# Kernel optimization log

Hardware: AMD Instinct MI355X
Metric: run time of the kernel (lower is better)

Reference implementation:

```python
import jax, jax.numpy as jnp
import numpy as np
from jax import lax

NUM_LAYERS = 3
NUM_QUBITS = 8
BATCH = 131072
DIM = 2 ** NUM_QUBITS  # 256


def _rot_mats(params):
    # params: (L, Q, 3) angles for RX, RY, RZ. Returns combined U = RZ @ RY @ RX, (L, Q, 2, 2) complex64.
    half = params * 0.5
    cx = jnp.cos(half[..., 0]).astype(jnp.complex64)
    sx = jnp.sin(half[..., 0]).astype(jnp.complex64)
    cy = jnp.cos(half[..., 1]).astype(jnp.complex64)
    sy = jnp.sin(half[..., 1]).astype(jnp.complex64)
    ezm = jnp.exp(-1j * half[..., 2]).astype(jnp.complex64)
    ezp = jnp.exp(1j * half[..., 2]).astype(jnp.complex64)
    zero = jnp.zeros_like(cx)
    RX = jnp.stack([jnp.stack([cx, -1j * sx], -1), jnp.stack([-1j * sx, cx], -1)], -2)
    RY = jnp.stack([jnp.stack([cy, -sy], -1), jnp.stack([sy, cy], -1)], -2)
    RZ = jnp.stack([jnp.stack([ezm, zero], -1), jnp.stack([zero, ezp], -1)], -2)
    return jnp.einsum('lqij,lqjk,lqkm->lqim', RZ, RY, RX)


def _apply_1q(state, U, wire):
    # state: (B, 2,2,...,2); wire w lives on axis w+1 (PennyLane wire 0 = most significant bit)
    ax = wire + 1
    return jnp.moveaxis(jnp.tensordot(U, state, axes=((1,), (ax,))), 0, ax)


def _apply_cnot(state, ctrl, tgt):
    c_ax, t_ax = ctrl + 1, tgt + 1
    s0 = lax.index_in_dim(state, 0, axis=c_ax, keepdims=True)
    s1 = lax.index_in_dim(state, 1, axis=c_ax, keepdims=True)
    s1 = jnp.flip(s1, axis=t_ax)
    return jnp.concatenate([s0, s1], axis=c_ax)


def _circuit(params, state_re, state_im):
    U = _rot_mats(params)  # (L, Q, 2, 2)
    state = (state_re + 1j * state_im).astype(jnp.complex64)
    state = state.reshape((state.shape[0],) + (2,) * NUM_QUBITS)
    for l in range(NUM_LAYERS):
        for q in range(NUM_QUBITS):
            state = _apply_1q(state, U[l, q], q)
        for q in range(NUM_QUBITS):
            state = _apply_cnot(state, q, (q + 1) % NUM_QUBITS)
    state = state.reshape(state.shape[0], DIM)
    # probability that wire 0 measures |0>: sum |amp|^2 over first half of amplitudes
    half = state[:, : DIM // 2]
    return jnp.sum(half.real ** 2 + half.imag ** 2, axis=1).astype(jnp.float32)


def setup_inputs() -> dict:
    key = jax.random.key(0)
    k1, k2, k3 = jax.random.split(key, 3)
    params = jax.random.uniform(k1, (NUM_LAYERS, NUM_QUBITS, 3), dtype=jnp.float32)
    sr = jax.random.normal(k2, (BATCH, DIM), dtype=jnp.float32)
    si = jax.random.normal(k3, (BATCH, DIM), dtype=jnp.float32)
    norm = jnp.sqrt(jnp.sum(sr ** 2 + si ** 2, axis=1, keepdims=True))
    return {"params": params, "state_re": sr / norm, "state_im": si / norm}


def reference(params, state_re, state_im):
    return _circuit(params, state_re, state_im)
```

## Files before the change

kernel.cpp:

```cpp
#include <hip/hip_runtime.h>
#include <stdint.h>

#define NLAYERS 3
#define NQ 8
#define DIM 256
#define BATCH 131072

typedef float  f32x4  __attribute__((ext_vector_type(4)));
typedef __bf16 bf16x8 __attribute__((ext_vector_type(8)));

__device__ __forceinline__ unsigned short f2bf(float f){
    union { float f; uint32_t u; } v; v.f = f;
    uint32_t u = v.u;
    u += 0x7fffu + ((u >> 16) & 1u);
    return (unsigned short)(u >> 16);
}

__device__ __forceinline__ float2 cmul(float2 a, float2 b){
    return make_float2(a.x*b.x - a.y*b.y, a.x*b.y + a.y*b.x);
}

__device__ __forceinline__ void gload_lds16(void* lds, const void* g){
    __builtin_amdgcn_global_load_lds(
        (const __attribute__((address_space(1))) unsigned int*)g,
        (__attribute__((address_space(3))) unsigned int*)lds,
        16, 0, 0);
}

__global__ __launch_bounds__(256) void build_w_kernel(const float* __restrict__ params,
                                                      unsigned short* __restrict__ W){
    __shared__ float2 st[2][DIM];
    __shared__ float2 gm[NLAYERS*NQ][4];
    const int j = blockIdx.x;
    const int i = threadIdx.x;

    if (i < NLAYERS*NQ){
        const float* pp = params + i*3;
        float hx = 0.5f*pp[0], hy = 0.5f*pp[1], hz = 0.5f*pp[2];
        float cx = cosf(hx), sx = sinf(hx);
        float cy = cosf(hy), sy = sinf(hy);
        float cz = cosf(hz), sz = sinf(hz);
        float2 ezm = make_float2(cz, -sz), ezp = make_float2(cz, sz);
        float2 m00 = make_float2( cy*cx,  sy*sx);
        float2 m01 = make_float2(-sy*cx, -cy*sx);
        float2 m10 = make_float2( sy*cx, -cy*sx);
        float2 m11 = make_float2( cy*cx, -sy*sx);
        gm[i][0] = cmul(ezm, m00);
        gm[i][1] = cmul(ezm, m01);
        gm[i][2] = cmul(ezp, m10);
        gm[i][3] = cmul(ezp, m11);
    }

    int psrc = i;
    #pragma unroll
    for (int q = NQ-1; q >= 0; --q){
        int c  = 7 - q;
        int tb = 7 - ((q + 1) & 7);
        psrc = ((psrc >> c) & 1) ? (psrc ^ (1 << tb)) : psrc;
    }

    int cur = 0;
    st[0][i] = make_float2(i == j ? 1.0f : 0.0f, 0.0f);
    __syncthreads();

    for (int l = 0; l < NLAYERS; ++l){
        for (int q = 0; q < NQ; ++q){
            float2 U0a = gm[l*NQ+q][0], U0b = gm[l*NQ+q][1];
            float2 U1a = gm[l*NQ+q][2], U1b = gm[l*NQ+q][3];
            int p  = 7 - q;
            int bs = (i >> p) & 1;
            int i0 = i & ~(1 << p), i1 = i | (1 << p);
            float2 a0 = st[cur][i0], a1 = st[cur][i1];
            float2 ua = bs ? U1a : U0a;
            float2 ub = bs ? U1b : U0b;
            float2 r;
            r.x = ua.x*a0.x - ua.y*a0.y + ub.x*a1.x - ub.y*a1.y;
            r.y = ua.x*a0.y + ua.y*a0.x + ub.x*a1.y + ub.y*a1.x;
            st[cur ^ 1][i] = r;
            cur ^= 1;
            __syncthreads();
        }
        float2 r = st[cur][psrc];
        st[cur ^ 1][i] = r;
        cur ^= 1;
        __syncthreads();
    }

    const int m = i & 127;
    float2 a = st[cur][m];
    if (i < 128) W[(uint32_t)m*256u + (uint32_t)j]          = f2bf(a.x);
    else         W[32768u + (uint32_t)m*256u + (uint32_t)j] = f2bf(a.y);
}


#define STAGE(B) { \
    gload_lds16(&Abuf[B][(c0+0)*DIM], srcp0); srcp0 += 16*DIM; \
    gload_lds16(&Abuf[B][(c0+1)*DIM], srcp1); srcp1 += 16*DIM; \
    gload_lds16(&Abuf[B][(c0+2)*DIM], srcp2); srcp2 += 16*DIM; \
    gload_lds16(&Abuf[B][(c0+3)*DIM], srcp3); srcp3 += 16*DIM; \
    gload_lds16(&Abuf[B][(c0+4)*DIM], srcp4); srcp4 += 16*DIM; \
    gload_lds16(&Abuf[B][(c0+5)*DIM], srcp5); srcp5 += 16*DIM; \
    gload_lds16(&Abuf[B][(c0+6)*DIM], srcp6); srcp6 += 16*DIM; \
    gload_lds16(&Abuf[B][(c0+7)*DIM], srcp7); srcp7 += 16*DIM; }

#define LOADB(F, S) \
    const bf16x8 bre_##F##_##S = *(const bf16x8*)(wrp##F + S*32); \
    const bf16x8 bim_##F##_##S = *(const bf16x8*)(wrp##F + 32768 + S*32);

#define BSTEP(S) { \
    f32x4 ra0 = *(const f32x4*)(arow + S*32 + o0); \
    f32x4 ra1 = *(const f32x4*)(arow + S*32 + o1); \
    f32x4 qa0 = *(const f32x4*)(irow + S*32 + o0); \
    f32x4 qa1 = *(const f32x4*)(irow + S*32 + o1); \
    union { f32x4 v; uint32_t u[4]; } ha_, hb_; \
    union { uint32_t u[4]; bf16x8 f; } pr_, pi_, pn_; \
    ha_.v = ra0; hb_.v = ra1; \
    pr_.u[0] = __builtin_amdgcn_perm(ha_.u[1], ha_.u[0], 0x07060302); \
    pr_.u[1] = __builtin_amdgcn_perm(ha_.u[3], ha_.u[2], 0x07060302); \
    pr_.u[2] = __builtin_amdgcn_perm(hb_.u[1], hb_.u[0], 0x07060302); \
    pr_.u[3] = __builtin_amdgcn_perm(hb_.u[3], hb_.u[2], 0x07060302); \
    ha_.v = qa0; hb_.v = qa1; \
    pi_.u[0] = __builtin_amdgcn_perm(ha_.u[1], ha_.u[0], 0x07060302); \
    pi_.u[1] = __builtin_amdgcn_perm(ha_.u[3], ha_.u[2], 0x07060302); \
    pi_.u[2] = __builtin_amdgcn_perm(hb_.u[1], hb_.u[0], 0x07060302); \
    pi_.u[3] = __builtin_amdgcn_perm(hb_.u[3], hb_.u[2], 0x07060302); \
    pn_.u[0] = pi_.u[0] ^ 0x80008000u; \
    pn_.u[1] = pi_.u[1] ^ 0x80008000u; \
    pn_.u[2] = pi_.u[2] ^ 0x80008000u; \
    pn_.u[3] = pi_.u[3] ^ 0x80008000u; \
    const bf16x8 fr_ = pr_.f, fi_ = pi_.f, fn_ = pn_.f; \
    accR0 = __builtin_amdgcn_mfma_f32_16x16x32_bf16(fr_, bre_0_##S, accR0, 0, 0, 0); \
    accR0 = __builtin_amdgcn_mfma_f32_16x16x32_bf16(fn_, bim_0_##S, accR0, 0, 0, 0); \
    accI0 = __builtin_amdgcn_mfma_f32_16x16x32_bf16(fr_, bim_0_##S, accI0, 0, 0, 0); \
    accI0 = __builtin_amdgcn_mfma_f32_16x16x32_bf16(fi_, bre_0_##S, accI0, 0, 0, 0); \
    accR1 = __builtin_amdgcn_mfma_f32_16x16x32_bf16(fr_, bre_1_##S, accR1, 0, 0, 0); \
    accR1 = __builtin_amdgcn_mfma_f32_16x16x32_bf16(fn_, bim_1_##S, accR1, 0, 0, 0); \
    accI1 = __builtin_amdgcn_mfma_f32_16x16x32_bf16(fr_, bim_1_##S, accI1, 0, 0, 0); \
    accI1 = __builtin_amdgcn_mfma_f32_16x16x32_bf16(fi_, bre_1_##S, accI1, 0, 0, 0); \
}

__global__ __launch_bounds__(256, 2) void qform4_kernel(const float* __restrict__ sr,
                                                        const float* __restrict__ si,
                                                        const unsigned short* __restrict__ W,
                                                        float* __restrict__ out){
    __shared__ float Abuf[2][32*DIM];
    __shared__ float red[64];

    const int tid  = threadIdx.x;
    const int lane = tid & 63;
    const int w    = tid >> 6;
    const int l15  = lane & 15;
    const int quad = lane >> 4;
    const int x7   = l15 & 7;
    const size_t m0 = (size_t)blockIdx.x * 128;

    const int c0 = w * 8;
    #define SRCP(I) ((((c0+I) < 16) ? sr : si) + (m0 + ((c0+I)&15))*DIM + ((lane ^ ((c0+I)&7)) << 2))
    const float* srcp0 = SRCP(0);
    const float* srcp1 = SRCP(1);
    const float* srcp2 = SRCP(2);
    const float* srcp3 = SRCP(3);
    const float* srcp4 = SRCP(4);
    const float* srcp5 = SRCP(5);
    const float* srcp6 = SRCP(6);
    const float* srcp7 = SRCP(7);
    #undef SRCP

    STAGE(0)

    const unsigned short* wrp0 = W + ((uint32_t)(w*32 +  0 + l15))*256u + (uint32_t)(quad*8);
    const unsigned short* wrp1 = W + ((uint32_t)(w*32 + 16 + l15))*256u + (uint32_t)(quad*8);
    LOADB(0,0) LOADB(0,1) LOADB(0,2) LOADB(0,3)
    LOADB(0,4) LOADB(0,5) LOADB(0,6) LOADB(0,7)
    LOADB(1,0) LOADB(1,1) LOADB(1,2) LOADB(1,3)
    LOADB(1,4) LOADB(1,5) LOADB(1,6) LOADB(1,7)

    const int o0 = (((quad << 1)    ) ^ x7) << 2;
    const int o1 = (((quad << 1) | 1) ^ x7) << 2;

    int buf = 0;
    #pragma unroll 1
    for (int t = 0; t < 8; ++t){
        if (t < 7){
            STAGE(buf ^ 1)
            asm volatile("s_waitcnt vmcnt(8)" ::: "memory");
        } else {
            asm volatile("s_waitcnt vmcnt(0)" ::: "memory");
        }
        __builtin_amdgcn_s_barrier();
        __builtin_amdgcn_sched_barrier(0);

        const float* arow = &Abuf[buf][l15 * DIM];
        const float* irow = &Abuf[buf][(16 + l15) * DIM];

        f32x4 accR0 = {0.f,0.f,0.f,0.f}, accI0 = {0.f,0.f,0.f,0.f};
        f32x4 accR1 = {0.f,0.f,0.f,0.f}, accI1 = {0.f,0.f,0.f,0.f};
        BSTEP(0) BSTEP(1) BSTEP(2) BSTEP(3)
        BSTEP(4) BSTEP(5) BSTEP(6) BSTEP(7)

        #pragma unroll
        for (int r = 0; r < 4; ++r){
            const float v0 = accR0[r], u0 = accI0[r];
            const float v1 = accR1[r], u1 = accI1[r];
            float tt = v0*v0 + u0*u0 + v1*v1 + u1*u1;
            tt += __shfl_xor(tt, 1);
            tt += __shfl_xor(tt, 2);
            tt += __shfl_xor(tt, 4);
            tt += __shfl_xor(tt, 8);
            if (l15 == 0) red[w*16 + quad*4 + r] = tt;
        }
        asm volatile("s_waitcnt lgkmcnt(0)" ::: "memory");
        __builtin_amdgcn_s_barrier();
        __builtin_amdgcn_sched_barrier(0);

        if (tid < 16){
            out[m0 + t*16 + tid] = red[tid] + red[16 + tid] + red[32 + tid] + red[48 + tid];
        }
        buf ^= 1;
    }
}

extern "C" void kernel_launch(void* const* d_in, const int* in_sizes, int n_in,
                              void* d_out, int out_size, void* d_ws, size_t ws_size,
                              hipStream_t stream){
    const float* params = (const float*)d_in[0];
    const float* sr     = (const float*)d_in[1];
    const float* si     = (const float*)d_in[2];
    unsigned short* Wimg = (unsigned short*)d_ws;
    float* out          = (float*)d_out;

    build_w_kernel<<<dim3(DIM), dim3(256), 0, stream>>>(params, Wimg);
    qform4_kernel<<<dim3(1024), dim3(256), 0, stream>>>(sr, si, Wimg, out);
}
```

Before: 301.8 us.

## Stage input tiles through registers and merge per-iteration barriers

Swaps the direct global-to-LDS async loads for ordinary vector loads into registers, which are then written to LDS after each compute step. The next tile's loads are issued one iteration ahead and land in the other LDS buffer. The reduction scratch array is double-buffered so each loop iteration needs only one workgroup barrier instead of two. The trade-off is extra VGPR pressure from holding eight float4 values per thread, plus explicit ds_write instructions in place of the hardware LDS-direct path.

```diff
diff --git a/kernel.cpp b/kernel.cpp
--- a/kernel.cpp
+++ b/kernel.cpp
@@ -18,13 +18,6 @@
 
 __device__ __forceinline__ float2 cmul(float2 a, float2 b){
     return make_float2(a.x*b.x - a.y*b.y, a.x*b.y + a.y*b.x);
-}
-
-__device__ __forceinline__ void gload_lds16(void* lds, const void* g){
-    __builtin_amdgcn_global_load_lds(
-        (const __attribute__((address_space(1))) unsigned int*)g,
-        (__attribute__((address_space(3))) unsigned int*)lds,
-        16, 0, 0);
 }
 
 __global__ __launch_bounds__(256) void build_w_kernel(const float* __restrict__ params,
@@ -93,15 +86,25 @@
 }
 
 
-#define STAGE(B) { \
-    gload_lds16(&Abuf[B][(c0+0)*DIM], srcp0); srcp0 += 16*DIM; \
-    gload_lds16(&Abuf[B][(c0+1)*DIM], srcp1); srcp1 += 16*DIM; \
-    gload_lds16(&Abuf[B][(c0+2)*DIM], srcp2); srcp2 += 16*DIM; \
-    gload_lds16(&Abuf[B][(c0+3)*DIM], srcp3); srcp3 += 16*DIM; \
-    gload_lds16(&Abuf[B][(c0+4)*DIM], srcp4); srcp4 += 16*DIM; \
-    gload_lds16(&Abuf[B][(c0+5)*DIM], srcp5); srcp5 += 16*DIM; \
-    gload_lds16(&Abuf[B][(c0+6)*DIM], srcp6); srcp6 += 16*DIM; \
-    gload_lds16(&Abuf[B][(c0+7)*DIM], srcp7); srcp7 += 16*DIM; }
+#define STAGE_ISSUE() { \
+    g0 = *(const f32x4*)srcp0; srcp0 += 16*DIM; \
+    g1 = *(const f32x4*)srcp1; srcp1 += 16*DIM; \
+    g2 = *(const f32x4*)srcp2; srcp2 += 16*DIM; \
+    g3 = *(const f32x4*)srcp3; srcp3 += 16*DIM; \
+    g4 = *(const f32x4*)srcp4; srcp4 += 16*DIM; \
+    g5 = *(const f32x4*)srcp5; srcp5 += 16*DIM; \
+    g6 = *(const f32x4*)srcp6; srcp6 += 16*DIM; \
+    g7 = *(const f32x4*)srcp7; srcp7 += 16*DIM; }
+
+#define DSWRITE(B) { \
+    *(f32x4*)(&Abuf[B][(c0+0)*DIM + (lane<<2)]) = g0; \
+    *(f32x4*)(&Abuf[B][(c0+1)*DIM + (lane<<2)]) = g1; \
+    *(f32x4*)(&Abuf[B][(c0+2)*DIM + (lane<<2)]) = g2; \
+    *(f32x4*)(&Abuf[B][(c0+3)*DIM + (lane<<2)]) = g3; \
+    *(f32x4*)(&Abuf[B][(c0+4)*DIM + (lane<<2)]) = g4; \
+    *(f32x4*)(&Abuf[B][(c0+5)*DIM + (lane<<2)]) = g5; \
+    *(f32x4*)(&Abuf[B][(c0+6)*DIM + (lane<<2)]) = g6; \
+    *(f32x4*)(&Abuf[B][(c0+7)*DIM + (lane<<2)]) = g7; }
 
 #define LOADB(F, S) \
     const bf16x8 bre_##F##_##S = *(const bf16x8*)(wrp##F + S*32); \
@@ -139,12 +142,12 @@
     accI1 = __builtin_amdgcn_mfma_f32_16x16x32_bf16(fi_, bre_1_##S, accI1, 0, 0, 0); \
 }
 
-__global__ __launch_bounds__(256, 2) void qform4_kernel(const float* __restrict__ sr,
+__global__ __launch_bounds__(256, 2) void qform5_kernel(const float* __restrict__ sr,
                                                         const float* __restrict__ si,
                                                         const unsigned short* __restrict__ W,
                                                         float* __restrict__ out){
     __shared__ float Abuf[2][32*DIM];
-    __shared__ float red[64];
+    __shared__ float red[2][64];
 
     const int tid  = threadIdx.x;
     const int lane = tid & 63;
@@ -166,7 +169,7 @@
     const float* srcp7 = SRCP(7);
     #undef SRCP
 
-    STAGE(0)
+    f32x4 g0, g1, g2, g3, g4, g5, g6, g7;
 
     const unsigned short* wrp0 = W + ((uint32_t)(w*32 +  0 + l15))*256u + (uint32_t)(quad*8);
     const unsigned short* wrp1 = W + ((uint32_t)(w*32 + 16 + l15))*256u + (uint32_t)(quad*8);
@@ -175,21 +178,20 @@
     LOADB(1,0) LOADB(1,1) LOADB(1,2) LOADB(1,3)
     LOADB(1,4) LOADB(1,5) LOADB(1,6) LOADB(1,7)
 
+    STAGE_ISSUE()
+    asm volatile("s_waitcnt vmcnt(0)" ::: "memory");
+    DSWRITE(0)
+    STAGE_ISSUE()
+    asm volatile("s_waitcnt lgkmcnt(0)" ::: "memory");
+    __builtin_amdgcn_s_barrier();
+    __builtin_amdgcn_sched_barrier(0);
+
     const int o0 = (((quad << 1)    ) ^ x7) << 2;
     const int o1 = (((quad << 1) | 1) ^ x7) << 2;
 
     int buf = 0;
     #pragma unroll 1
     for (int t = 0; t < 8; ++t){
-        if (t < 7){
-            STAGE(buf ^ 1)
-            asm volatile("s_waitcnt vmcnt(8)" ::: "memory");
-        } else {
-            asm volatile("s_waitcnt vmcnt(0)" ::: "memory");
-        }
-        __builtin_amdgcn_s_barrier();
-        __builtin_amdgcn_sched_barrier(0);
-
         const float* arow = &Abuf[buf][l15 * DIM];
         const float* irow = &Abuf[buf][(16 + l15) * DIM];
 
@@ -207,14 +209,21 @@
             tt += __shfl_xor(tt, 2);
             tt += __shfl_xor(tt, 4);
             tt += __shfl_xor(tt, 8);
-            if (l15 == 0) red[w*16 + quad*4 + r] = tt;
+            if (l15 == 0) red[t & 1][w*16 + quad*4 + r] = tt;
+        }
+
+        if (t < 7){
+            asm volatile("s_waitcnt vmcnt(0)" ::: "memory");
+            DSWRITE(buf ^ 1)
+            if (t < 6) STAGE_ISSUE()
         }
         asm volatile("s_waitcnt lgkmcnt(0)" ::: "memory");
         __builtin_amdgcn_s_barrier();
         __builtin_amdgcn_sched_barrier(0);
 
         if (tid < 16){
-            out[m0 + t*16 + tid] = red[tid] + red[16 + tid] + red[32 + tid] + red[48 + tid];
+            const float* rd = red[t & 1];
+            out[m0 + t*16 + tid] = rd[tid] + rd[16 + tid] + rd[32 + tid] + rd[48 + tid];
         }
         buf ^= 1;
     }
@@ -230,5 +239,5 @@
     float* out          = (float*)d_out;
 
     build_w_kernel<<<dim3(DIM), dim3(256), 0, stream>>>(params, Wimg);
-    qform4_kernel<<<dim3(1024), dim3(256), 0, stream>>>(sr, si, Wimg, out);
-}
+    qform5_kernel<<<dim3(1024), dim3(256), 0, stream>>>(sr, si, Wimg, out);
+}
```

Result: no change. 297.4 us (-1.5%).
